# Kernel tuning notes

Hardware: AMD Instinct MI355X
Metric: run time of the kernel (lower is better)

## Reference

```python
import jax, jax.numpy as jnp
import numpy as np
from jax import lax

BN_EPS = 1e-5

def _conv1d_same(x, w):
    # x: [N, 1, C], w: [1, 1, k] with k odd -> SAME padding along channel axis
    k = w.shape[-1]
    return lax.conv_general_dilated(x, w, window_strides=(1,),
                                    padding=[(k // 2, k // 2)],
                                    dimension_numbers=('NCH', 'OIH', 'NCH'))

def setup_inputs() -> dict:
    key = jax.random.key(0)
    ks = jax.random.split(key, 6)
    B, C, H, W = 4, 64, 64, 64
    kk = 3  # kernel size from in_dim=64: t=int(abs(log2(64)+1)/2)=3 (odd)
    x = jax.random.normal(ks[0], (B, C, H, W), dtype=jnp.float32)
    q_w = jax.random.normal(ks[1], (1, 1, kk), dtype=jnp.float32) * 0.5
    k_w = jax.random.normal(ks[2], (1, 1, kk), dtype=jnp.float32) * 0.5
    v_w = jax.random.normal(ks[3], (C, C), dtype=jnp.float32) * (1.0 / np.sqrt(C))
    v_b = jnp.zeros((C,), dtype=jnp.float32)
    gamma = jax.random.uniform(ks[4], (1,), dtype=jnp.float32, minval=0.5, maxval=1.5)
    bn_w = jnp.ones((C,), dtype=jnp.float32)
    bn_b = jnp.zeros((C,), dtype=jnp.float32)
    return {"x": x, "q_w": q_w, "k_w": k_w, "v_w": v_w, "v_b": v_b,
            "gamma": gamma, "bn_w": bn_w, "bn_b": bn_b}

def reference(x, q_w, k_w, v_w, v_b, gamma, bn_w, bn_b):
    B, C, H, W = x.shape
    N = H * W
    # conv1d Q/K projections over the channel axis, per spatial position
    xp = x.reshape(B, C, N).transpose(0, 2, 1).reshape(B * N, 1, C)
    q = _conv1d_same(xp, q_w).reshape(B, N, C)   # proj_query: [B, HW, C]
    k = _conv1d_same(xp, k_w).reshape(B, N, C)   # proj_key (pre-permute)
    energy = jnp.einsum('bnc,bmc->bnm', q, k)    # [B, HW, HW]
    attn = jax.nn.softmax(energy, axis=-1)
    # 1x1 value conv
    v = jnp.einsum('oc,bchw->bohw', v_w, x) + v_b[None, :, None, None]
    vv = v.reshape(B, C, N)
    # bmm(value, attention^T)
    out = jnp.einsum('bcm,bnm->bcn', vv, attn).reshape(B, C, H, W)
    y = gamma[0] * out
    # BatchNorm2d, training mode (batch statistics, biased variance)
    mean = jnp.mean(y, axis=(0, 2, 3), keepdims=True)
    var = jnp.var(y, axis=(0, 2, 3), keepdims=True)
    y = (y - mean) * lax.rsqrt(var + BN_EPS)
    y = y * bn_w[None, :, None, None] + bn_b[None, :, None, None]
    return y + x
```

## Files before the change

### kernel.cpp

```cpp
#include <hip/hip_runtime.h>
#include <stdint.h>

using f16 = _Float16;

typedef _Float16 f16x8 __attribute__((ext_vector_type(8)));
typedef float f32x4 __attribute__((ext_vector_type(4)));

#define LOG2E 1.44269504088896340736f

__device__ __forceinline__ f16 f2h(float f) { return (f16)f; }

#if __has_builtin(__builtin_amdgcn_exp2f)
__device__ __forceinline__ float fexp2(float x) { return __builtin_amdgcn_exp2f(x); }
#else
__device__ __forceinline__ float fexp2(float x) { return exp2f(x); }
#endif

__device__ __forceinline__ f16x8 cvt8(const float* p) {
  const float4 a = *(const float4*)p;
  const float4 b = *(const float4*)(p + 4);
  f16x8 r;
  r[0] = (f16)a.x; r[1] = (f16)a.y; r[2] = (f16)a.z; r[3] = (f16)a.w;
  r[4] = (f16)b.x; r[5] = (f16)b.y; r[6] = (f16)b.z; r[7] = (f16)b.w;
  return r;
}


__global__ __launch_bounds__(256, 1) void pam_pre(
    const float* __restrict__ x, const float* __restrict__ qw,
    const float* __restrict__ kw, const float* __restrict__ vw,
    const float* __restrict__ vb,
    f16* __restrict__ qa, f16* __restrict__ ka, f16* __restrict__ va)
{
  __shared__ alignas(16) f16 xt[64 * 72];
  const int tid = threadIdx.x;
  const int b = blockIdx.x >> 6;
  const int n0 = (blockIdx.x & 63) << 6;
  const int lane = tid & 63;
  const int wv = tid >> 6;
  const int quad = lane >> 4, l15 = lane & 15;

  for (int p = 0; p < 4; ++p) {
    const int c = p * 16 + (tid >> 4);
    const int j0 = (tid & 15) << 2;
    const float4 v4 = *(const float4*)(x + ((size_t)(b * 64 + c) << 12) + n0 + j0);
    xt[(j0 + 0) * 72 + c] = f2h(v4.x);
    xt[(j0 + 1) * 72 + c] = f2h(v4.y);
    xt[(j0 + 2) * 72 + c] = f2h(v4.z);
    xt[(j0 + 3) * 72 + c] = f2h(v4.w);
  }
  __syncthreads();

  const float qw0 = qw[0], qw1 = qw[1], qw2 = qw[2];
  const float kw0 = kw[0], kw1 = kw[1], kw2 = kw[2];
  for (int p = 0; p < 16; ++p) {
    const int c = lane;
    const int jr = (p << 2) + wv;
    const int n = n0 + jr;
    const float xm = (c > 0) ? (float)xt[jr * 72 + c - 1] : 0.f;
    const float x0 = (float)xt[jr * 72 + c];
    const float xp = (c < 63) ? (float)xt[jr * 72 + c + 1] : 0.f;
    const float qv = (qw0 * xm + qw1 * x0 + qw2 * xp) * LOG2E;
    const float kv = kw0 * xm + kw1 * x0 + kw2 * xp;
    const size_t off = ((size_t)((b << 12) + n) << 6) + c;
    qa[off] = f2h(qv);
    ka[off] = f2h(kv);
  }

  {
    const f16x8 a0 = cvt8(vw + (wv * 16 + l15) * 64 + quad * 8);
    const f16x8 a1 = cvt8(vw + (wv * 16 + l15) * 64 + quad * 8 + 32);
    f32x4 acc[4];
    for (int st = 0; st < 4; ++st) {
      const f16x8 b0 = *(const f16x8*)&xt[(st * 16 + l15) * 72 + quad * 8];
      const f16x8 b1 = *(const f16x8*)&xt[(st * 16 + l15) * 72 + quad * 8 + 32];
      f32x4 z = {0.f, 0.f, 0.f, 0.f};
      z = __builtin_amdgcn_mfma_f32_16x16x32_f16(a0, b0, z, 0, 0, 0);
      acc[st] = __builtin_amdgcn_mfma_f32_16x16x32_f16(a1, b1, z, 0, 0, 0);
    }
    const int cobase = wv * 16 + quad * 4;
    for (int st = 0; st < 4; ++st)
      for (int r = 0; r < 4; ++r) {
        const int co = cobase + r;
        const float val = acc[st][r] + vb[co];
        va[((size_t)(b * 64 + co) << 12) + n0 + st * 16 + l15] = f2h(val);
      }
  }
}

__global__ __launch_bounds__(256, 2) void pam_attn(
    const f16* __restrict__ qa, const f16* __restrict__ ka,
    const f16* __restrict__ va, const float* __restrict__ gam,
    float* __restrict__ y0, float* __restrict__ gs1, float* __restrict__ gs2)
{
  __shared__ alignas(16) f16 pbuf[4][32 * 32];
  __shared__ float ldsO[32 * 65];
  __shared__ float ldsL[4][32];
  __shared__ float ldsM[4][32];
  __shared__ float ldsInv[32];

  const int tid = threadIdx.x;
  const int wv = tid >> 6, lane = tid & 63;
  const int quad = lane >> 4, l15 = lane & 15;
  const int b = blockIdx.x & 3;
  const int qt_idx = blockIdx.x >> 2;
  const int qb0 = qt_idx << 5;
  const int phase = qt_idx & 31;

  for (int i = tid; i < 32 * 65; i += 256) ldsO[i] = 0.f;

  const int bn = b << 12;
  f16x8 bq[2][2];
  for (int qt = 0; qt < 2; ++qt) {
    const int q = qb0 + qt * 16 + l15;
    const f16* qp = qa + ((size_t)(bn + q) << 6) + quad * 8;
    bq[qt][0] = *(const f16x8*)qp;
    bq[qt][1] = *(const f16x8*)(qp + 32);
  }

  f32x4 o[2][4] = {};
  float m[2] = {-1e30f, -1e30f};
  float lpart[2] = {0.f, 0.f};
  f16* pb = pbuf[wv];

  f16x8 ak[2][2], bv[4];
  {
    const int kb = (phase << 7) + wv * 32;
    for (int mt = 0; mt < 2; ++mt) {
      const f16* kp = ka + ((size_t)(bn + kb + mt * 16 + l15) << 6) + quad * 8;
      ak[mt][0] = *(const f16x8*)kp;
      ak[mt][1] = *(const f16x8*)(kp + 32);
    }
    for (int ct = 0; ct < 4; ++ct)
      bv[ct] = *(const f16x8*)(va + ((size_t)(b * 64 + ct * 16 + l15) << 12) + kb + quad * 8);
  }

#pragma unroll 1
  for (int kt = 0; kt < 32; ++kt) {
    f16x8 akn[2][2], bvn[4];
    {
      const int kb2 = ((((kt + 1) + phase) & 31) << 7) + wv * 32;
      for (int mt = 0; mt < 2; ++mt) {
        const f16* kp = ka + ((size_t)(bn + kb2 + mt * 16 + l15) << 6) + quad * 8;
        akn[mt][0] = *(const f16x8*)kp;
        akn[mt][1] = *(const f16x8*)(kp + 32);
      }
      for (int ct = 0; ct < 4; ++ct)
        bvn[ct] = *(const f16x8*)(va + ((size_t)(b * 64 + ct * 16 + l15) << 12) + kb2 + quad * 8);
    }

    for (int qt = 0; qt < 2; ++qt) {
      f32x4 s[2];
      for (int mt = 0; mt < 2; ++mt) {
        f32x4 z = {0.f, 0.f, 0.f, 0.f};
        z = __builtin_amdgcn_mfma_f32_16x16x32_f16(ak[mt][0], bq[qt][0], z, 0, 0, 0);
        s[mt] = __builtin_amdgcn_mfma_f32_16x16x32_f16(ak[mt][1], bq[qt][1], z, 0, 0, 0);
      }
      float tmax = fmaxf(fmaxf(fmaxf(s[0][0], s[0][1]), fmaxf(s[0][2], s[0][3])),
                         fmaxf(fmaxf(s[1][0], s[1][1]), fmaxf(s[1][2], s[1][3])));
      tmax = fmaxf(tmax, __shfl_xor(tmax, 16, 64));
      tmax = fmaxf(tmax, __shfl_xor(tmax, 32, 64));
      const float mnew = fmaxf(m[qt], tmax);
      const float alpha = fexp2(m[qt] - mnew);
      m[qt] = mnew;

      const int rowq = qt * 16 + l15;
      char* rowp = (char*)pb + rowq * 64;
      const int sw = rowq & 3;
      float tsum = 0.f;
      for (int mt = 0; mt < 2; ++mt) {
        const float p0 = fexp2(s[mt][0] - mnew);
        const float p1 = fexp2(s[mt][1] - mnew);
        const float p2 = fexp2(s[mt][2] - mnew);
        const float p3 = fexp2(s[mt][3] - mnew);
        tsum += (p0 + p1) + (p2 + p3);
        union { f16 h[4]; uint2 u; } pk;
        pk.h[0] = f2h(p0); pk.h[1] = f2h(p1);
        pk.h[2] = f2h(p2); pk.h[3] = f2h(p3);
        const int cc = (2 * mt + (quad >> 1)) ^ sw;
        *(uint2*)(rowp + cc * 16 + (quad & 1) * 8) = pk.u;
      }
      lpart[qt] = lpart[qt] * alpha + tsum;

      const int srcbase = (lane & 48) + ((lane >> 4) << 2);
      for (int r = 0; r < 4; ++r) {
        const float ar = __shfl(alpha, srcbase + r, 64);
        for (int ct = 0; ct < 4; ++ct) o[qt][ct][r] *= ar;
      }
    }
    __builtin_amdgcn_s_waitcnt(0xC07F);

    for (int qt = 0; qt < 2; ++qt) {
      const int rowq = qt * 16 + l15;
      const f16x8 ap =
          *(const f16x8*)((const char*)pb + rowq * 64 + ((quad ^ (rowq & 3)) << 4));
      for (int ct = 0; ct < 4; ++ct)
        o[qt][ct] = __builtin_amdgcn_mfma_f32_16x16x32_f16(ap, bv[ct], o[qt][ct], 0, 0, 0);
    }

    for (int mt = 0; mt < 2; ++mt) { ak[mt][0] = akn[mt][0]; ak[mt][1] = akn[mt][1]; }
    for (int ct = 0; ct < 4; ++ct) bv[ct] = bvn[ct];
  }

  for (int qt = 0; qt < 2; ++qt) {
    float v = lpart[qt];
    v += __shfl_xor(v, 16, 64);
    v += __shfl_xor(v, 32, 64);
    if (quad == 0) {
      ldsM[wv][qt * 16 + l15] = m[qt];
      ldsL[wv][qt * 16 + l15] = v;
    }
  }
  __syncthreads();

  for (int qt = 0; qt < 2; ++qt) {
    for (int r = 0; r < 4; ++r) {
      const int q = qt * 16 + quad * 4 + r;
      const float M = fmaxf(fmaxf(ldsM[0][q], ldsM[1][q]),
                            fmaxf(ldsM[2][q], ldsM[3][q]));
      const float sc = fexp2(ldsM[wv][q] - M);
      for (int ct = 0; ct < 4; ++ct)
        atomicAdd(&ldsO[q * 65 + ct * 16 + l15], o[qt][ct][r] * sc);
    }
  }
  __syncthreads();
  if (tid < 32) {
    const int q = tid;
    const float M = fmaxf(fmaxf(ldsM[0][q], ldsM[1][q]),
                          fmaxf(ldsM[2][q], ldsM[3][q]));
    const float lt = ldsL[0][q] * fexp2(ldsM[0][q] - M) +
                     ldsL[1][q] * fexp2(ldsM[1][q] - M) +
                     ldsL[2][q] * fexp2(ldsM[2][q] - M) +
                     ldsL[3][q] * fexp2(ldsM[3][q] - M);
    ldsInv[q] = 1.f / lt;
  }
  __syncthreads();

  const float g = gam[0];
  {
    const int c = tid >> 2;
    const int q0 = (tid & 3) << 3;
    float s1 = 0.f, s2 = 0.f;
    float4 v4a, v4b;
    float* va4 = &v4a.x;
    float* vb4 = &v4b.x;
    for (int r = 0; r < 4; ++r) {
      const float val = g * ldsO[(q0 + r) * 65 + c] * ldsInv[q0 + r];
      va4[r] = val; s1 += val; s2 += val * val;
    }
    for (int r = 0; r < 4; ++r) {
      const float val = g * ldsO[(q0 + 4 + r) * 65 + c] * ldsInv[q0 + 4 + r];
      vb4[r] = val; s1 += val; s2 += val * val;
    }
    float* dst = y0 + ((size_t)(b * 64 + c) << 12) + qb0 + q0;
    *(float4*)dst = v4a;
    *(float4*)(dst + 4) = v4b;
    s1 += __shfl_xor(s1, 1, 64);
    s2 += __shfl_xor(s2, 1, 64);
    s1 += __shfl_xor(s1, 2, 64);
    s2 += __shfl_xor(s2, 2, 64);
    if ((tid & 3) == 0) {
      atomicAdd(&gs1[c], s1);
      atomicAdd(&gs2[c], s2);
    }
  }
}

__global__ __launch_bounds__(64, 1) void pam_stats(
    const float* __restrict__ gs1, const float* __restrict__ gs2,
    const float* __restrict__ bnw, const float* __restrict__ bnb,
    float2* __restrict__ par)
{
  const int c = threadIdx.x;
  const float inv_n = 1.f / 16384.f;
  const float mean = gs1[c] * inv_n;
  const float var = fmaxf(gs2[c] * inv_n - mean * mean, 0.f);
  const float sc = bnw[c] * rsqrtf(var + 1e-5f);
  par[c] = make_float2(sc, bnb[c] - mean * sc);
}

__global__ __launch_bounds__(256, 1) void pam_apply(
    const float* __restrict__ y0, const float* __restrict__ x,
    const float2* __restrict__ par, float* __restrict__ out)
{
  const int i = (blockIdx.x * 256 + threadIdx.x) << 2;
  const int c = (i >> 12) & 63;
  const float2 p = par[c];
  const float4 y = *(const float4*)(y0 + i);
  const float4 xv = *(const float4*)(x + i);
  float4 r;
  r.x = y.x * p.x + p.y + xv.x;
  r.y = y.y * p.x + p.y + xv.y;
  r.z = y.z * p.x + p.y + xv.z;
  r.w = y.w * p.x + p.y + xv.w;
  *(float4*)(out + i) = r;
}

extern "C" void kernel_launch(void* const* d_in, const int* in_sizes, int n_in,
                              void* d_out, int out_size, void* d_ws, size_t ws_size,
                              hipStream_t stream)
{
  (void)in_sizes; (void)n_in; (void)out_size; (void)ws_size;
  const float* x   = (const float*)d_in[0];
  const float* qw  = (const float*)d_in[1];
  const float* kw  = (const float*)d_in[2];
  const float* vw  = (const float*)d_in[3];
  const float* vb  = (const float*)d_in[4];
  const float* gam = (const float*)d_in[5];
  const float* bnw = (const float*)d_in[6];
  const float* bnb = (const float*)d_in[7];

  char* ws = (char*)d_ws;
  f16*   qa  = (f16*)(ws);
  f16*   ka  = (f16*)(ws + (2u << 20));
  f16*   va  = (f16*)(ws + (4u << 20));
  float* y0  = (float*)(ws + (6u << 20));
  char*  st  = ws + (10u << 20);
  float*  gs1  = (float*)(st);
  float*  gs2  = (float*)(st + 256);
  float2* par  = (float2*)(st + 512);

  hipMemsetAsync(st, 0, 512, stream);
  pam_pre  <<<256, 256, 0, stream>>>(x, qw, kw, vw, vb, qa, ka, va);
  pam_attn <<<512, 256, 0, stream>>>(qa, ka, va, gam, y0, gs1, gs2);
  pam_stats<<<1, 64, 0, stream>>>(gs1, gs2, bnw, bnb, par);
  pam_apply<<<1024, 256, 0, stream>>>(y0, x, par, (float*)d_out);
}
```

Before: 170.3 us.

## Widen attention blocks to 8 waves, halve pre tiles, fuse stats and memset

Result: slower. 237.8 us (+39.6%).

```diff
diff --git a/kernel.cpp b/kernel.cpp
--- a/kernel.cpp
+++ b/kernel.cpp
@@ -26,34 +26,43 @@
 }
 
 
-__global__ __launch_bounds__(256, 1) void pam_pre(
+__global__ __launch_bounds__(256, 2) void pam_pre(
     const float* __restrict__ x, const float* __restrict__ qw,
     const float* __restrict__ kw, const float* __restrict__ vw,
     const float* __restrict__ vb,
-    f16* __restrict__ qa, f16* __restrict__ ka, f16* __restrict__ va)
+    f16* __restrict__ qa, f16* __restrict__ ka, f16* __restrict__ va,
+    float* __restrict__ gz)
 {
-  __shared__ alignas(16) f16 xt[64 * 72];
+  __shared__ alignas(16) f16 xt[32 * 72];
   const int tid = threadIdx.x;
-  const int b = blockIdx.x >> 6;
-  const int n0 = (blockIdx.x & 63) << 6;
+  const int b = blockIdx.x >> 7;
+  const int n0 = (blockIdx.x & 127) << 5;
   const int lane = tid & 63;
   const int wv = tid >> 6;
   const int quad = lane >> 4, l15 = lane & 15;
 
-  for (int p = 0; p < 4; ++p) {
-    const int c = p * 16 + (tid >> 4);
-    const int j0 = (tid & 15) << 2;
-    const float4 v4 = *(const float4*)(x + ((size_t)(b * 64 + c) << 12) + n0 + j0);
-    xt[(j0 + 0) * 72 + c] = f2h(v4.x);
-    xt[(j0 + 1) * 72 + c] = f2h(v4.y);
-    xt[(j0 + 2) * 72 + c] = f2h(v4.z);
-    xt[(j0 + 3) * 72 + c] = f2h(v4.w);
+  if (blockIdx.x == 0 && tid < 128) gz[tid] = 0.f;
+
+  {
+    const int c = tid >> 2;
+    const int j0 = (tid & 3) << 3;
+    const float* xp = x + ((size_t)(b * 64 + c) << 12) + n0 + j0;
+    const float4 v0 = *(const float4*)xp;
+    const float4 v1 = *(const float4*)(xp + 4);
+    xt[(j0 + 0) * 72 + c] = f2h(v0.x);
+    xt[(j0 + 1) * 72 + c] = f2h(v0.y);
+    xt[(j0 + 2) * 72 + c] = f2h(v0.z);
+    xt[(j0 + 3) * 72 + c] = f2h(v0.w);
+    xt[(j0 + 4) * 72 + c] = f2h(v1.x);
+    xt[(j0 + 5) * 72 + c] = f2h(v1.y);
+    xt[(j0 + 6) * 72 + c] = f2h(v1.z);
+    xt[(j0 + 7) * 72 + c] = f2h(v1.w);
   }
   __syncthreads();
 
   const float qw0 = qw[0], qw1 = qw[1], qw2 = qw[2];
   const float kw0 = kw[0], kw1 = kw[1], kw2 = kw[2];
-  for (int p = 0; p < 16; ++p) {
+  for (int p = 0; p < 8; ++p) {
     const int c = lane;
     const int jr = (p << 2) + wv;
     const int n = n0 + jr;
@@ -70,8 +79,8 @@
   {
     const f16x8 a0 = cvt8(vw + (wv * 16 + l15) * 64 + quad * 8);
     const f16x8 a1 = cvt8(vw + (wv * 16 + l15) * 64 + quad * 8 + 32);
-    f32x4 acc[4];
-    for (int st = 0; st < 4; ++st) {
+    f32x4 acc[2];
+    for (int st = 0; st < 2; ++st) {
       const f16x8 b0 = *(const f16x8*)&xt[(st * 16 + l15) * 72 + quad * 8];
       const f16x8 b1 = *(const f16x8*)&xt[(st * 16 + l15) * 72 + quad * 8 + 32];
       f32x4 z = {0.f, 0.f, 0.f, 0.f};
@@ -79,7 +88,7 @@
       acc[st] = __builtin_amdgcn_mfma_f32_16x16x32_f16(a1, b1, z, 0, 0, 0);
     }
     const int cobase = wv * 16 + quad * 4;
-    for (int st = 0; st < 4; ++st)
+    for (int st = 0; st < 2; ++st)
       for (int r = 0; r < 4; ++r) {
         const int co = cobase + r;
         const float val = acc[st][r] + vb[co];
@@ -88,15 +97,16 @@
   }
 }
 
-__global__ __launch_bounds__(256, 2) void pam_attn(
+__global__ __launch_bounds__(512, 4) void pam_attn(
     const f16* __restrict__ qa, const f16* __restrict__ ka,
     const f16* __restrict__ va, const float* __restrict__ gam,
     float* __restrict__ y0, float* __restrict__ gs1, float* __restrict__ gs2)
 {
-  __shared__ alignas(16) f16 pbuf[4][32 * 32];
+  __shared__ alignas(16) f16 pbuf[8][32 * 32];
   __shared__ float ldsO[32 * 65];
-  __shared__ float ldsL[4][32];
-  __shared__ float ldsM[4][32];
+  __shared__ float ldsL[8][32];
+  __shared__ float ldsM[8][32];
+  __shared__ float ldsMg[32];
   __shared__ float ldsInv[32];
 
   const int tid = threadIdx.x;
@@ -105,9 +115,9 @@
   const int b = blockIdx.x & 3;
   const int qt_idx = blockIdx.x >> 2;
   const int qb0 = qt_idx << 5;
-  const int phase = qt_idx & 31;
-
-  for (int i = tid; i < 32 * 65; i += 256) ldsO[i] = 0.f;
+  const int phase = qt_idx & 15;
+
+  for (int i = tid; i < 32 * 65; i += 512) ldsO[i] = 0.f;
 
   const int bn = b << 12;
   f16x8 bq[2][2];
@@ -125,7 +135,7 @@
 
   f16x8 ak[2][2], bv[4];
   {
-    const int kb = (phase << 7) + wv * 32;
+    const int kb = (phase << 8) + wv * 32;
     for (int mt = 0; mt < 2; ++mt) {
       const f16* kp = ka + ((size_t)(bn + kb + mt * 16 + l15) << 6) + quad * 8;
       ak[mt][0] = *(const f16x8*)kp;
@@ -136,10 +146,10 @@
   }
 
 #pragma unroll 1
-  for (int kt = 0; kt < 32; ++kt) {
+  for (int kt = 0; kt < 16; ++kt) {
     f16x8 akn[2][2], bvn[4];
     {
-      const int kb2 = ((((kt + 1) + phase) & 31) << 7) + wv * 32;
+      const int kb2 = ((((kt + 1) + phase) & 15) << 8) + wv * 32;
       for (int mt = 0; mt < 2; ++mt) {
         const f16* kp = ka + ((size_t)(bn + kb2 + mt * 16 + l15) << 6) + quad * 8;
         akn[mt][0] = *(const f16x8*)kp;
@@ -213,86 +223,72 @@
   }
   __syncthreads();
 
+  if (tid < 32) {
+    const int q = tid;
+    float M = ldsM[0][q];
+    for (int w = 1; w < 8; ++w) M = fmaxf(M, ldsM[w][q]);
+    float lt = 0.f;
+    for (int w = 0; w < 8; ++w) lt += ldsL[w][q] * fexp2(ldsM[w][q] - M);
+    ldsMg[q] = M;
+    ldsInv[q] = 1.f / lt;
+  }
+  __syncthreads();
+
   for (int qt = 0; qt < 2; ++qt) {
     for (int r = 0; r < 4; ++r) {
       const int q = qt * 16 + quad * 4 + r;
-      const float M = fmaxf(fmaxf(ldsM[0][q], ldsM[1][q]),
-                            fmaxf(ldsM[2][q], ldsM[3][q]));
-      const float sc = fexp2(ldsM[wv][q] - M);
+      const float sc = fexp2(ldsM[wv][q] - ldsMg[q]);
       for (int ct = 0; ct < 4; ++ct)
         atomicAdd(&ldsO[q * 65 + ct * 16 + l15], o[qt][ct][r] * sc);
     }
   }
   __syncthreads();
-  if (tid < 32) {
-    const int q = tid;
-    const float M = fmaxf(fmaxf(ldsM[0][q], ldsM[1][q]),
-                          fmaxf(ldsM[2][q], ldsM[3][q]));
-    const float lt = ldsL[0][q] * fexp2(ldsM[0][q] - M) +
-                     ldsL[1][q] * fexp2(ldsM[1][q] - M) +
-                     ldsL[2][q] * fexp2(ldsM[2][q] - M) +
-                     ldsL[3][q] * fexp2(ldsM[3][q] - M);
-    ldsInv[q] = 1.f / lt;
-  }
-  __syncthreads();
 
   const float g = gam[0];
   {
-    const int c = tid >> 2;
-    const int q0 = (tid & 3) << 3;
+    const int c = tid >> 3;
+    const int q0 = (tid & 7) << 2;
+    float4 v4;
+    float* vp = &v4.x;
     float s1 = 0.f, s2 = 0.f;
-    float4 v4a, v4b;
-    float* va4 = &v4a.x;
-    float* vb4 = &v4b.x;
     for (int r = 0; r < 4; ++r) {
       const float val = g * ldsO[(q0 + r) * 65 + c] * ldsInv[q0 + r];
-      va4[r] = val; s1 += val; s2 += val * val;
-    }
-    for (int r = 0; r < 4; ++r) {
-      const float val = g * ldsO[(q0 + 4 + r) * 65 + c] * ldsInv[q0 + 4 + r];
-      vb4[r] = val; s1 += val; s2 += val * val;
-    }
-    float* dst = y0 + ((size_t)(b * 64 + c) << 12) + qb0 + q0;
-    *(float4*)dst = v4a;
-    *(float4*)(dst + 4) = v4b;
+      vp[r] = val; s1 += val; s2 += val * val;
+    }
+    *(float4*)(y0 + ((size_t)(b * 64 + c) << 12) + qb0 + q0) = v4;
     s1 += __shfl_xor(s1, 1, 64);
     s2 += __shfl_xor(s2, 1, 64);
     s1 += __shfl_xor(s1, 2, 64);
     s2 += __shfl_xor(s2, 2, 64);
-    if ((tid & 3) == 0) {
+    s1 += __shfl_xor(s1, 4, 64);
+    s2 += __shfl_xor(s2, 4, 64);
+    if ((tid & 7) == 0) {
       atomicAdd(&gs1[c], s1);
       atomicAdd(&gs2[c], s2);
     }
   }
 }
 
-__global__ __launch_bounds__(64, 1) void pam_stats(
+__global__ __launch_bounds__(256, 4) void pam_apply(
+    const float* __restrict__ y0, const float* __restrict__ x,
     const float* __restrict__ gs1, const float* __restrict__ gs2,
     const float* __restrict__ bnw, const float* __restrict__ bnb,
-    float2* __restrict__ par)
+    float* __restrict__ out)
 {
-  const int c = threadIdx.x;
+  const int i = (blockIdx.x * 256 + threadIdx.x) << 2;
+  const int c = (i >> 12) & 63;
   const float inv_n = 1.f / 16384.f;
   const float mean = gs1[c] * inv_n;
   const float var = fmaxf(gs2[c] * inv_n - mean * mean, 0.f);
   const float sc = bnw[c] * rsqrtf(var + 1e-5f);
-  par[c] = make_float2(sc, bnb[c] - mean * sc);
-}
-
-__global__ __launch_bounds__(256, 1) void pam_apply(
-    const float* __restrict__ y0, const float* __restrict__ x,
-    const float2* __restrict__ par, float* __restrict__ out)
-{
-  const int i = (blockIdx.x * 256 + threadIdx.x) << 2;
-  const int c = (i >> 12) & 63;
-  const float2 p = par[c];
+  const float sh = bnb[c] - mean * sc;
   const float4 y = *(const float4*)(y0 + i);
   const float4 xv = *(const float4*)(x + i);
   float4 r;
-  r.x = y.x * p.x + p.y + xv.x;
-  r.y = y.y * p.x + p.y + xv.y;
-  r.z = y.z * p.x + p.y + xv.z;
-  r.w = y.w * p.x + p.y + xv.w;
+  r.x = y.x * sc + sh + xv.x;
+  r.y = y.y * sc + sh + xv.y;
+  r.z = y.z * sc + sh + xv.z;
+  r.w = y.w * sc + sh + xv.w;
   *(float4*)(out + i) = r;
 }
 
@@ -315,14 +311,10 @@
   f16*   ka  = (f16*)(ws + (2u << 20));
   f16*   va  = (f16*)(ws + (4u << 20));
   float* y0  = (float*)(ws + (6u << 20));
-  char*  st  = ws + (10u << 20);
-  float*  gs1  = (float*)(st);
-  float*  gs2  = (float*)(st + 256);
-  float2* par  = (float2*)(st + 512);
-
-  hipMemsetAsync(st, 0, 512, stream);
-  pam_pre  <<<256, 256, 0, stream>>>(x, qw, kw, vw, vb, qa, ka, va);
-  pam_attn <<<512, 256, 0, stream>>>(qa, ka, va, gam, y0, gs1, gs2);
-  pam_stats<<<1, 64, 0, stream>>>(gs1, gs2, bnw, bnb, par);
-  pam_apply<<<1024, 256, 0, stream>>>(y0, x, par, (float*)d_out);
-}
+  float* gs1 = (float*)(ws + (10u << 20));
+  float* gs2 = (float*)(ws + (10u << 20) + 256);
+
+  pam_pre  <<<512, 256, 0, stream>>>(x, qw, kw, vw, vb, qa, ka, va, gs1);
+  pam_attn <<<512, 512, 0, stream>>>(qa, ka, va, gam, y0, gs1, gs2);
+  pam_apply<<<1024, 256, 0, stream>>>(y0, x, gs1, gs2, bnw, bnb, (float*)d_out);
+}
```
